# Performance work log

Hardware: AMD Instinct MI355X
Metric: run time of the kernel (lower is better)

Reference implementation:

```python
import jax, jax.numpy as jnp
import numpy as np

N_HEAD = 16


def setup_inputs() -> dict:
    key = jax.random.key(0)
    k1, k2, k3 = jax.random.split(key, 3)
    B, T, C = 4, 2048, 2048
    x = jax.random.normal(k1, (B, T, C), dtype=jnp.float32)
    # weights stored as [in, out] so y = x @ W + b (equivalent to torch Linear)
    w_attn = jax.random.normal(k2, (C, 3 * C), dtype=jnp.float32) * 0.02
    b_attn = jnp.zeros((3 * C,), dtype=jnp.float32)
    w_proj = jax.random.normal(k3, (C, C), dtype=jnp.float32) * 0.02
    b_proj = jnp.zeros((C,), dtype=jnp.float32)
    return {"x": x, "w_attn": w_attn, "b_attn": b_attn, "w_proj": w_proj, "b_proj": b_proj}


def reference(x, w_attn, b_attn, w_proj, b_proj):
    B, T, C = x.shape
    H = N_HEAD
    D = C // H
    qkv = x @ w_attn + b_attn                     # [B,T,3C]
    q, k, v = jnp.split(qkv, 3, axis=-1)
    q = q.reshape(B, T, H, D).transpose(0, 2, 1, 3)  # [B,H,T,D]
    k = k.reshape(B, T, H, D).transpose(0, 2, 1, 3)
    v = v.reshape(B, T, H, D).transpose(0, 2, 1, 3)
    att = jnp.einsum("bhqd,bhkd->bhqk", q, k) * (1.0 / jnp.sqrt(jnp.float32(D)))
    causal = jnp.tril(jnp.ones((T, T), dtype=bool))
    att = jnp.where(causal[None, None], att, jnp.float32(-jnp.inf))
    att = jax.nn.softmax(att, axis=-1)
    y = jnp.einsum("bhqk,bhkd->bhqd", att, v)     # [B,H,T,D]
    y = y.transpose(0, 2, 1, 3).reshape(B, T, C)
    return y @ w_proj + b_proj
```

## Files before the change

### kernel.cpp

```cpp
#include <hip/hip_runtime.h>
#include <cstdint>

typedef unsigned short u16;
typedef u16   u16x4 __attribute__((ext_vector_type(4)));
typedef u16   u16x8 __attribute__((ext_vector_type(8)));
typedef short s16x8 __attribute__((ext_vector_type(8)));
typedef float f32x4 __attribute__((ext_vector_type(4)));

__device__ __forceinline__ u16 f2bf(float f) {
  union { float f; unsigned u; } v; v.f = f;
  unsigned u = v.u;
  return (u16)((u + 0x7fffu + ((u >> 16) & 1u)) >> 16);
}

__device__ __forceinline__ void gld_lds16(const u16* g, u16* l) {
  __builtin_amdgcn_global_load_lds((const __attribute__((address_space(1))) void*)g,
                                   (__attribute__((address_space(3))) void*)l, 16, 0, 0);
}

__device__ __forceinline__ void transpose_cast_body(
    const float* __restrict__ in, u16* __restrict__ outp, int R, int Cin,
    int cx, int cy, u16 (*tile)[72]) {
  const int c0 = cx * 64, r0 = cy * 64;
  const int t = threadIdx.x;
  const int r = t >> 2, cs = (t & 3) * 16;
  const float* src = in + (size_t)(r0 + r) * Cin + c0 + cs;
#pragma unroll
  for (int q = 0; q < 4; ++q) {
    float4 v = *(const float4*)(src + q * 4);
    tile[r][cs + q * 4 + 0] = f2bf(v.x);
    tile[r][cs + q * 4 + 1] = f2bf(v.y);
    tile[r][cs + q * 4 + 2] = f2bf(v.z);
    tile[r][cs + q * 4 + 3] = f2bf(v.w);
  }
  __syncthreads();
  u16x8 w0, w1;
#pragma unroll
  for (int q = 0; q < 8; ++q) { w0[q] = tile[cs + q][r]; w1[q] = tile[cs + 8 + q][r]; }
  u16* dst = outp + (size_t)(c0 + r) * R + r0 + cs;
  *(u16x8*)dst = w0;
  *(u16x8*)(dst + 8) = w1;
}

__global__ void prep_k(const float* __restrict__ x, u16* __restrict__ xb,
                       const float* __restrict__ w_attn, u16* __restrict__ waT,
                       const float* __restrict__ w_proj, u16* __restrict__ wpT) {
  __shared__ u16 tile[64][72];
  const int bx = blockIdx.x;
  if (bx < 8192) {
    size_t i = ((size_t)bx * 256 + threadIdx.x) * 8;
    float4 a = *(const float4*)(x + i);
    float4 b = *(const float4*)(x + i + 4);
    u16x8 r;
    r[0] = f2bf(a.x); r[1] = f2bf(a.y); r[2] = f2bf(a.z); r[3] = f2bf(a.w);
    r[4] = f2bf(b.x); r[5] = f2bf(b.y); r[6] = f2bf(b.z); r[7] = f2bf(b.w);
    *(u16x8*)(xb + i) = r;
  } else if (bx < 11264) {
    int idx = bx - 8192;
    transpose_cast_body(w_attn, waT, 2048, 6144, idx % 96, idx / 96, tile);
  } else {
    int idx = bx - 11264;
    transpose_cast_body(w_proj, wpT, 2048, 2048, idx % 32, idx / 32, tile);
  }
}

template <int EPI>
__global__ __launch_bounds__(512, 2) void gemm256(
    const u16* __restrict__ A, const u16* __restrict__ Bt,
    const float* __restrict__ bias,
    u16* __restrict__ o0, u16* __restrict__ o1, u16* __restrict__ o2,
    float* __restrict__ ofp, int Ntiles, int Kdim) {
  __shared__ __align__(128) u16 sm[65536];
  const int nwg = gridDim.x;
  const int orig = blockIdx.x;
  const int qq = nwg >> 3;
  const int bid = (orig & 7) * qq + (orig >> 3);
  const int mt = bid / Ntiles, nt = bid % Ntiles;
  const int tid = threadIdx.x, lane = tid & 63, wave = tid >> 6;
  const int wr = wave >> 2, wc = wave & 3;
  const int l15 = lane & 15, lhi = lane >> 4;
  f32x4 acc[8][4] = {};
  const int nK = Kdim >> 6;

#define VMA(n) asm volatile("s_waitcnt vmcnt(" n ")" ::: "memory")
#define BARK   asm volatile("s_barrier" ::: "memory")
#define DSA(qm)                                                                          \
  do {                                                                                   \
    _Pragma("unroll") for (int mi = 0; mi < 4; ++mi)                                     \
    _Pragma("unroll") for (int kk = 0; kk < 2; ++kk)                                     \
      af[mi * 2 + kk] = *(const s16x8*)&sm[(size_t)(cA + (qm) * 1024 +                   \
          (kk * 4 + lhi) * 128 + wr * 64 + mi * 16 + l15) * 8];                          \
  } while (0)
#define DSB(dst, qn)                                                                     \
  do {                                                                                   \
    _Pragma("unroll") for (int ni = 0; ni < 2; ++ni)                                     \
    _Pragma("unroll") for (int kk = 0; kk < 2; ++kk)                                     \
      dst[ni * 2 + kk] = *(const s16x8*)&sm[(size_t)(cB + (qn) * 1024 +                  \
          (kk * 4 + lhi) * 128 + wc * 32 + ni * 16 + l15) * 8];                          \
  } while (0)
#define STA(qm, k0, sbase)                                                               \
  do {                                                                                   \
    _Pragma("unroll") for (int l = 0; l < 2; ++l)                                        \
      gld_lds16(A + (size_t)(mt * 256 + (wave & 1) * 128 + (qm) * 64 + lane) * Kdim +    \
                    (k0) + (l * 4 + (wave >> 1)) * 8,                                    \
                &sm[(size_t)((sbase) + (qm) * 1024 + l * 512 + wave * 64) * 8]);         \
  } while (0)
#define STB(qn, k0, sbase)                                                               \
  do {                                                                                   \
    _Pragma("unroll") for (int l = 0; l < 2; ++l)                                        \
      gld_lds16(Bt + (size_t)(nt * 256 + ((wave & 1) * 2 + (lane >> 5)) * 64 +           \
                              (qn) * 32 + (lane & 31)) * Kdim +                          \
                     (k0) + (l * 4 + (wave >> 1)) * 8,                                   \
                &sm[(size_t)((sbase) + (qn) * 1024 + l * 512 + wave * 64) * 8]);         \
  } while (0)
#define MM(qm, qn, BF)                                                                   \
  do {                                                                                   \
    __builtin_amdgcn_s_setprio(1);                                                       \
    _Pragma("unroll") for (int mi = 0; mi < 4; ++mi)                                     \
    _Pragma("unroll") for (int ni = 0; ni < 2; ++ni)                                     \
    _Pragma("unroll") for (int kk = 0; kk < 2; ++kk)                                     \
      acc[(qm) * 4 + mi][(qn) * 2 + ni] = __builtin_amdgcn_mfma_f32_16x16x32_bf16(       \
          af[mi * 2 + kk], BF[ni * 2 + kk], acc[(qm) * 4 + mi][(qn) * 2 + ni], 0, 0, 0); \
    __builtin_amdgcn_s_setprio(0);                                                       \
  } while (0)
#define TILE(t, DO1, DO2, V0, V1, V3)                                                    \
  do {                                                                                   \
    const int cA = ((t) & 1) * 2048, cB = 4096 + ((t) & 1) * 2048;                       \
    const int sA1 = (((t) + 1) & 1) * 2048;                                              \
    const int sA2 = ((t) & 1) * 2048, sB2 = 4096 + ((t) & 1) * 2048;                     \
    const int k1 = ((t) + 1) << 6, k2 = ((t) + 2) << 6;                                  \
    s16x8 af[8], bf0[4], bf1[4];                                                         \
                                                                                \
    DSA(0); DSB(bf0, 0);                                                                 \
    if (DO1) STA(1, k1, sA1);                                                            \
    VMA(V0); BARK; MM(0, 0, bf0); BARK;                                                  \
                                                                                \
    DSB(bf1, 1);                                                                         \
    if (DO2) STA(0, k2, sA2);                                                            \
    VMA(V1); BARK; MM(0, 1, bf1); BARK;                                                  \
                                                                                \
    DSA(1);                                                                              \
    if (DO2) STB(0, k2, sB2);                                                            \
    BARK; MM(1, 1, bf1); BARK;                                                           \
                                                                                \
    if (DO2) STB(1, k2, sB2);                                                            \
    if (DO1) VMA(V3);                                                                    \
    BARK; MM(1, 0, bf0); BARK;                                                           \
  } while (0)

  STA(0, 0, 0); STB(0, 0, 4096); STB(1, 0, 4096); STA(1, 0, 0);
  STA(0, 64, 2048); STB(0, 64, 6144); STB(1, 64, 6144);
  VMA("10");
  BARK;

  for (int t = 0; t < nK - 2; ++t) TILE(t, true, true, "10", "10", "10");
  TILE(nK - 2, true, false, "10", "8", "4");
  TILE(nK - 1, false, false, "2", "0", "0");

#undef VMA
#undef BARK
#undef DSA
#undef DSB
#undef STA
#undef STB
#undef MM
#undef TILE

  const int row0 = mt * 256 + wr * 128;
  const int col0 = nt * 256 + wc * 64;
  float bcol[4];
#pragma unroll
  for (int ni = 0; ni < 4; ++ni) bcol[ni] = bias[col0 + ni * 16 + l15];
  if constexpr (EPI == 0) {
#pragma unroll
    for (int ni = 0; ni < 4; ++ni) {
      int cc = col0 + ni * 16 + l15;
      int which = cc >> 11, h = (cc >> 7) & 15, d = cc & 127;
      if (which == 2) {
#pragma unroll
        for (int mi = 0; mi < 8; ++mi) {
          int t0 = row0 + mi * 16 + lhi * 4;
          int bb = t0 >> 11, tt = t0 & 2047;
          u16x4 w;
#pragma unroll
          for (int j = 0; j < 4; ++j) w[j] = f2bf(acc[mi][ni][j] + bcol[ni]);
          *(u16x4*)&o2[(((size_t)bb * 16 + h) * 128 + d) * 2048 + tt] = w;
        }
      } else {
        u16* o = (which == 0) ? o0 : o1;
#pragma unroll
        for (int mi = 0; mi < 8; ++mi)
#pragma unroll
          for (int j = 0; j < 4; ++j) {
            int row = row0 + mi * 16 + lhi * 4 + j;
            int bb = row >> 11, tt = row & 2047;
            o[(((size_t)bb * 16 + h) * 2048 + tt) * 128 + d] = f2bf(acc[mi][ni][j] + bcol[ni]);
          }
      }
    }
  } else {
#pragma unroll
    for (int mi = 0; mi < 8; ++mi)
#pragma unroll
      for (int j = 0; j < 4; ++j) {
        int row = row0 + mi * 16 + lhi * 4 + j;
#pragma unroll
        for (int ni = 0; ni < 4; ++ni)
          ofp[(size_t)row * 2048 + col0 + ni * 16 + l15] = acc[mi][ni][j] + bcol[ni];
      }
  }
}

__global__ __launch_bounds__(512, 4) void attn_k(
    const u16* __restrict__ Q, const u16* __restrict__ Kg,
    const u16* __restrict__ Vt, u16* __restrict__ Y) {
  __shared__ u16 Ks[8192];
  __shared__ u16 Vs[8192];
  __shared__ u16 Ps[8][16 * 72];
  const int p = blockIdx.x, bh = blockIdx.y;
  const int tid = threadIdx.x, lane = tid & 63, wave = tid >> 6;
  const int l15 = lane & 15, lhi = lane >> 4;
  const size_t bhT = (size_t)bh * 2048;
  const int b = bh >> 4, h = bh & 15;
  const float sc = 0.08838834764831845f * 1.4426950408889634f;

  for (int hf = 0; hf < 2; ++hf) {
    const int qt = hf ? 15 - p : p;
    const int r0 = qt * 128 + wave * 16;
    const int last = 2 * qt + 1;

    s16x8 qf[4];
#pragma unroll
    for (int kk = 0; kk < 4; ++kk)
      qf[kk] = *(const s16x8*)&Q[(bhT + r0 + l15) * 128 + kk * 32 + lhi * 8];

    f32x4 o[8] = {};
    float m_[4], l_[4];
#pragma unroll
    for (int j = 0; j < 4; ++j) { m_[j] = -1e30f; l_[j] = 0.f; }

    __syncthreads();
#pragma unroll
    for (int c = 0; c < 2; ++c) {
      int ci = c * 512 + tid;
      int dhi = ci >> 6, key = ci & 63;
      gld_lds16(Kg + (bhT + key) * 128 + dhi * 8, &Ks[(c * 512 + wave * 64) * 8]);
      int khi = ci >> 7, d = ci & 127;
      gld_lds16(Vt + ((size_t)bh * 128 + d) * 2048 + khi * 8, &Vs[(c * 512 + wave * 64) * 8]);
    }
    __syncthreads();

    for (int it = 0; it <= last; ++it) {
      const int j0 = it * 64;
      const bool have_next = (it < last);
      u16x8 kpre[2], vpre[2];
      if (have_next) {
        const int j1 = j0 + 64;
#pragma unroll
        for (int c = 0; c < 2; ++c) {
          int ci = c * 512 + tid;
          int dhi = ci >> 6, key = ci & 63;
          kpre[c] = *(const u16x8*)&Kg[(bhT + j1 + key) * 128 + dhi * 8];
          int khi = ci >> 7, d = ci & 127;
          vpre[c] = *(const u16x8*)&Vt[((size_t)bh * 128 + d) * 2048 + j1 + khi * 8];
        }
      }

      if (j0 <= r0 + 15) {
        f32x4 s[4] = {};
#pragma unroll
        for (int nc = 0; nc < 4; ++nc)
#pragma unroll
          for (int kk = 0; kk < 4; ++kk) {
            s16x8 kf = *(const s16x8*)&Ks[((kk * 4 + lhi) * 64 + nc * 16 + l15) * 8];
            s[nc] = __builtin_amdgcn_mfma_f32_16x16x32_bf16(qf[kk], kf, s[nc], 0, 0, 0);
          }
        const bool maskt = (j0 + 63 > r0);
        float rmax[4];
#pragma unroll
        for (int j = 0; j < 4; ++j) rmax[j] = -1e30f;
#pragma unroll
        for (int nc = 0; nc < 4; ++nc)
#pragma unroll
          for (int j = 0; j < 4; ++j) {
            float v = s[nc][j] * sc;
            if (maskt && (j0 + nc * 16 + l15) > (r0 + lhi * 4 + j)) v = -1e30f;
            s[nc][j] = v;
            rmax[j] = fmaxf(rmax[j], v);
          }
#pragma unroll
        for (int off = 1; off < 16; off <<= 1)
#pragma unroll
          for (int j = 0; j < 4; ++j) rmax[j] = fmaxf(rmax[j], __shfl_xor(rmax[j], off));

        float al[4], rsum[4];
#pragma unroll
        for (int j = 0; j < 4; ++j) {
          float mn = fmaxf(m_[j], rmax[j]);
          al[j] = exp2f(m_[j] - mn);
          m_[j] = mn;
          rsum[j] = 0.f;
        }
#pragma unroll
        for (int nc = 0; nc < 4; ++nc)
#pragma unroll
          for (int j = 0; j < 4; ++j) {
            float pv = exp2f(s[nc][j] - m_[j]);
            rsum[j] += pv;
            Ps[wave][(lhi * 4 + j) * 72 + nc * 16 + l15] = f2bf(pv);
          }
#pragma unroll
        for (int off = 1; off < 16; off <<= 1)
#pragma unroll
          for (int j = 0; j < 4; ++j) rsum[j] += __shfl_xor(rsum[j], off);
#pragma unroll
        for (int j = 0; j < 4; ++j) l_[j] = l_[j] * al[j] + rsum[j];
#pragma unroll
        for (int di = 0; di < 8; ++di)
#pragma unroll
          for (int j = 0; j < 4; ++j) o[di][j] *= al[j];

#pragma unroll
        for (int kk2 = 0; kk2 < 2; ++kk2) {
          s16x8 pf = *(const s16x8*)&Ps[wave][l15 * 72 + kk2 * 32 + lhi * 8];
#pragma unroll
          for (int di = 0; di < 8; ++di) {
            s16x8 vf = *(const s16x8*)&Vs[((kk2 * 4 + lhi) * 128 + di * 16 + l15) * 8];
            o[di] = __builtin_amdgcn_mfma_f32_16x16x32_bf16(pf, vf, o[di], 0, 0, 0);
          }
        }
      }

      if (have_next) {
        __syncthreads();
#pragma unroll
        for (int c = 0; c < 2; ++c) {
          *(u16x8*)&Ks[(c * 512 + tid) * 8] = kpre[c];
          *(u16x8*)&Vs[(c * 512 + tid) * 8] = vpre[c];
        }
        __syncthreads();
      }
    }

    float rl[4];
#pragma unroll
    for (int j = 0; j < 4; ++j) rl[j] = 1.0f / l_[j];
#pragma unroll
    for (int di = 0; di < 8; ++di)
#pragma unroll
      for (int j = 0; j < 4; ++j) {
        int row = b * 2048 + r0 + lhi * 4 + j;
        int col = h * 128 + di * 16 + l15;
        Y[(size_t)row * 2048 + col] = f2bf(o[di][j] * rl[j]);
      }
  }
}

extern "C" void kernel_launch(void* const* d_in, const int* in_sizes, int n_in,
                              void* d_out, int out_size, void* d_ws, size_t ws_size,
                              hipStream_t stream) {
  const float* x      = (const float*)d_in[0];
  const float* w_attn = (const float*)d_in[1];
  const float* b_attn = (const float*)d_in[2];
  const float* w_proj = (const float*)d_in[3];
  const float* b_proj = (const float*)d_in[4];
  float* out = (float*)d_out;

  char* ws = (char*)d_ws;
  u16* xb  = (u16*)(ws);
  u16* waT = (u16*)(ws + 33554432ull);
  u16* wpT = (u16*)(ws + 58720256ull);
  u16* Qb  = (u16*)(ws + 67108864ull);
  u16* Kb  = (u16*)(ws + 100663296ull);
  u16* Vtb = (u16*)(ws + 167772160ull);
  u16* Yb  = xb;

  prep_k<<<12288, 256, 0, stream>>>(x, xb, w_attn, waT, w_proj, wpT);
  gemm256<0><<<32 * 24, 512, 0, stream>>>(xb, waT, b_attn, Qb, Kb, Vtb, nullptr, 24, 2048);
  attn_k<<<dim3(8, 64), 512, 0, stream>>>(Qb, Kb, Vtb, Yb);
  gemm256<1><<<32 * 8, 512, 0, stream>>>(Yb, wpT, b_proj, nullptr, nullptr, nullptr, out, 8, 2048);
}
```

Baseline: 558.0 us.

## Restructure GEMM K-loop into lagged software pipeline with one-tile prefetch

Reworks the bf16 GEMM main loop so the last MFMA quadrant of each K-tile is deferred into the next tile, keeping fragments in ping-pong registers (afB, bf0e/bf0o). Prefetch depth drops from two tiles ahead to one, and the global-to-LDS loads are reordered so they issue earlier relative to the LDS reads they feed. The goal is to hide the LDS-read and barrier latency behind MFMA work, at the cost of more live registers and less memory latency hiding from the shallower prefetch.

```diff
diff --git a/kernel.cpp b/kernel.cpp
--- a/kernel.cpp
+++ b/kernel.cpp
@@ -84,11 +84,11 @@
 
 #define VMA(n) asm volatile("s_waitcnt vmcnt(" n ")" ::: "memory")
 #define BARK   asm volatile("s_barrier" ::: "memory")
-#define DSA(qm)                                                                          \
+#define DSA(dst, qm)                                                                     \
   do {                                                                                   \
     _Pragma("unroll") for (int mi = 0; mi < 4; ++mi)                                     \
     _Pragma("unroll") for (int kk = 0; kk < 2; ++kk)                                     \
-      af[mi * 2 + kk] = *(const s16x8*)&sm[(size_t)(cA + (qm) * 1024 +                   \
+      dst[mi * 2 + kk] = *(const s16x8*)&sm[(size_t)(cA + (qm) * 1024 +                  \
           (kk * 4 + lhi) * 128 + wr * 64 + mi * 16 + l15) * 8];                          \
   } while (0)
 #define DSB(dst, qn)                                                                     \
@@ -113,49 +113,56 @@
                      (k0) + (l * 4 + (wave >> 1)) * 8,                                   \
                 &sm[(size_t)((sbase) + (qn) * 1024 + l * 512 + wave * 64) * 8]);         \
   } while (0)
-#define MM(qm, qn, BF)                                                                   \
+#define MM(qm, qn, AF, BF)                                                               \
   do {                                                                                   \
     __builtin_amdgcn_s_setprio(1);                                                       \
     _Pragma("unroll") for (int mi = 0; mi < 4; ++mi)                                     \
     _Pragma("unroll") for (int ni = 0; ni < 2; ++ni)                                     \
     _Pragma("unroll") for (int kk = 0; kk < 2; ++kk)                                     \
       acc[(qm) * 4 + mi][(qn) * 2 + ni] = __builtin_amdgcn_mfma_f32_16x16x32_bf16(       \
-          af[mi * 2 + kk], BF[ni * 2 + kk], acc[(qm) * 4 + mi][(qn) * 2 + ni], 0, 0, 0); \
+          AF[mi * 2 + kk], BF[ni * 2 + kk], acc[(qm) * 4 + mi][(qn) * 2 + ni], 0, 0, 0); \
     __builtin_amdgcn_s_setprio(0);                                                       \
   } while (0)
-#define TILE(t, DO1, DO2, V0, V1, V3)                                                    \
-  do {                                                                                   \
-    const int cA = ((t) & 1) * 2048, cB = 4096 + ((t) & 1) * 2048;                       \
-    const int sA1 = (((t) + 1) & 1) * 2048;                                              \
-    const int sA2 = ((t) & 1) * 2048, sB2 = 4096 + ((t) & 1) * 2048;                     \
-    const int k1 = ((t) + 1) << 6, k2 = ((t) + 2) << 6;                                  \
-    s16x8 af[8], bf0[4], bf1[4];                                                         \
-                                                                                \
-    DSA(0); DSB(bf0, 0);                                                                 \
-    if (DO1) STA(1, k1, sA1);                                                            \
-    VMA(V0); BARK; MM(0, 0, bf0); BARK;                                                  \
-                                                                                \
+#define TILEP(t, PAR, CUR, PRV, DO1, V0, V1, LAG)                                        \
+  do {                                                                                   \
+    const int cA = (PAR) * 2048, cB = 4096 + (PAR) * 2048;                               \
+    const int sN = ((PAR) ^ 1) * 2048, sBN = 4096 + ((PAR) ^ 1) * 2048;                  \
+    const int k1 = ((t) + 1) << 6;                                                       \
+                             \
+    DSA(afA, 0); DSB(CUR, 0);                                                            \
+    if (DO1) STA(0, k1, sN);                                                             \
+    VMA(V0); BARK;                                                                       \
+    if (LAG) MM(1, 0, afB, PRV);                                                         \
+    BARK;                                                                                \
+                                         \
     DSB(bf1, 1);                                                                         \
-    if (DO2) STA(0, k2, sA2);                                                            \
-    VMA(V1); BARK; MM(0, 1, bf1); BARK;                                                  \
-                                                                                \
-    DSA(1);                                                                              \
-    if (DO2) STB(0, k2, sB2);                                                            \
-    BARK; MM(1, 1, bf1); BARK;                                                           \
-                                                                                \
-    if (DO2) STB(1, k2, sB2);                                                            \
-    if (DO1) VMA(V3);                                                                    \
-    BARK; MM(1, 0, bf0); BARK;                                                           \
-  } while (0)
+    if (DO1) STB(0, k1, sBN);                                                            \
+    VMA(V1); BARK;                                                                       \
+    MM(0, 0, afA, CUR); BARK;                                                            \
+                                         \
+    DSA(afB, 1);                                                                         \
+    if (DO1) STB(1, k1, sBN);                                                            \
+    BARK; MM(0, 1, afA, bf1); BARK;                                                      \
+                                                      \
+    if (DO1) STA(1, k1, sN);                                                             \
+    BARK; MM(1, 1, afB, bf1); BARK;                                                      \
+  } while (0)
+
+  s16x8 afA[8], afB[8], bf1[4], bf0e[4], bf0o[4];
 
   STA(0, 0, 0); STB(0, 0, 4096); STB(1, 0, 4096); STA(1, 0, 0);
-  STA(0, 64, 2048); STB(0, 64, 6144); STB(1, 64, 6144);
-  VMA("10");
+  VMA("4");
   BARK;
 
-  for (int t = 0; t < nK - 2; ++t) TILE(t, true, true, "10", "10", "10");
-  TILE(nK - 2, true, false, "10", "8", "4");
-  TILE(nK - 1, false, false, "2", "0", "0");
+  TILEP(0, 0, bf0e, bf0o, true, "4", "4", false);
+  TILEP(1, 1, bf0o, bf0e, true, "4", "4", true);
+  for (int t = 2; t < nK - 2; t += 2) {
+    TILEP(t, 0, bf0e, bf0o, true, "4", "4", true);
+    TILEP(t + 1, 1, bf0o, bf0e, true, "4", "4", true);
+  }
+  TILEP(nK - 2, 0, bf0e, bf0o, true, "4", "4", true);
+  TILEP(nK - 1, 1, bf0o, bf0e, false, "2", "0", true);
+  MM(1, 0, afB, bf0o);
 
 #undef VMA
 #undef BARK
@@ -164,7 +171,7 @@
 #undef STA
 #undef STB
 #undef MM
-#undef TILE
+#undef TILEP
 
   const int row0 = mt * 256 + wr * 128;
   const int col0 = nt * 256 + wc * 64;
```

Result: slower. 856.6 us (+53.5%).
